# Kernel optimization log

Measured on AMD Instinct MI355X. Metric: run time of the kernel, lower is better.

The kernel has to match this reference:

```python
import jax, jax.numpy as jnp
import numpy as np

SHAPE0 = (256, 256)   # top pyramid level (h, w)
SIGMA = 3.0
EPS = 1e-3
BATCH = 128
N_CHAN = 3
N_LEVELS = 4
N_PIX = sum((SHAPE0[0] >> i) * (SHAPE0[1] >> i) for i in range(N_LEVELS))  # 87040


def _gauss_lum_kernel(sigma):
    # 2D Gaussian times RGB luminance weights -> HWIO kernel (kh, kw, 3, 1)
    s = int(np.ceil(2 * sigma))
    u = np.linspace(-s, s, 2 * s + 1)
    g = np.exp(-(u[:, None] ** 2 + u[None, :] ** 2) / (2 * sigma ** 2)) / (2 * np.pi * sigma ** 2)
    w = np.array([0.2989, 0.587, 0.114])
    k = (g[:, :, None, None] * w[None, None, :, None]).astype(np.float32)
    return jnp.asarray(k)


def _conv_same(x, k):
    # NHWC conv with zero 'SAME' padding; equivalent to the original
    # pad(s) + SAME conv + center crop (net effect is SAME with zero pad).
    return jax.lax.conv_general_dilated(
        x, k, window_strides=(1, 1), padding='SAME',
        dimension_numbers=('NHWC', 'HWIO', 'NHWC'))


def setup_inputs() -> dict:
    key = jax.random.key(0)
    x = jax.random.uniform(key, (BATCH, N_PIX, N_CHAN), dtype=jnp.float32)
    return {"x": x}


def reference(x):
    k = _gauss_lum_kernel(SIGMA)
    n_pix, nc = x.shape[1], x.shape[2]
    h, w = SHAPE0
    outs = []
    i = 0
    while i + h * w <= n_pix:  # static Python loop over pyramid levels
        xi = x[:, i:i + h * w, :].reshape(-1, h, w, nc)          # (B,h,w,3)
        lum = _conv_same(xi, k)                                   # (B,h,w,1)
        dens = _conv_same(jnp.ones((1, h, w, nc), x.dtype), k)    # (1,h,w,1), input-independent
        outs.append((xi / (lum / dens + EPS)).reshape(-1, h * w, nc))
        i += h * w
        h //= 2
        w //= 2
    return jnp.concatenate(outs, axis=1)  # packed pyramid (B, n_pix, 3)
```

## Files before the change

kernel.cpp:

```cpp
#include <hip/hip_runtime.h>


#define NPIX   87040
#define EPSV   1e-3f
#define WSUM   0.9999f
#define TW     64
#define TH     16
#define RAD    6
#define LW     80
#define LWP    84
#define RCP    68
#define LH     28
#define NG     (LH * 20)
#define NBLK   11008
#define NXCD   8
#define CHUNK  (NBLK / NXCD)

__device__ __constant__ float G1[13] = {
    0.01799699f, 0.03315904f, 0.05467002f, 0.08065689f, 0.10648267f,
    0.12579441f, 0.13298076f, 0.12579441f, 0.10648267f, 0.08065689f,
    0.05467002f, 0.03315904f, 0.01799699f
};
__device__ __constant__ float PRE[14] = {
    0.00000000f, 0.01799699f, 0.05115603f, 0.10582605f, 0.18648294f,
    0.29296561f, 0.41876002f, 0.55174078f, 0.67753519f, 0.78401786f,
    0.86467475f, 0.91934477f, 0.95250381f, 0.97050080f
};

__global__ __launch_bounds__(256)
void mslln_kernel(const float* __restrict__ x, float* __restrict__ out) {
    __shared__ float s_mem[LH * LWP];
    __shared__ float s_rc[LH][RCP];
    float (*s_lum)[LWP]   = (float(*)[LWP])s_mem;
    float (*s_scale)[RCP] = (float(*)[RCP])s_mem;

    const int bphys = blockIdx.x;
    const int bid   = (bphys & (NXCD - 1)) * CHUNK + (bphys >> 3);
    const int t     = threadIdx.x;

    int img, tl, txlog, h, off;
    if (bid < 8192)       { img = bid >> 6;                 tl = bid & 63; txlog = 2; h = 256; off = 0;     }
    else if (bid < 10240) { int r = bid - 8192;  img = r >> 4; tl = r & 15; txlog = 1; h = 128; off = 65536; }
    else if (bid < 10752) { int r = bid - 10240; img = r >> 2; tl = r & 3;  txlog = 0; h = 64;  off = 81920; }
    else                  { int r = bid - 10752; img = r >> 1; tl = r & 1;  txlog = 0; h = 32;  off = 86016; }
    const int w   = h;
    const int tx0 = (tl & ((1 << txlog) - 1)) << 6;
    const int ty0 = (tl >> txlog) << 4;

    const float* __restrict__ xb = x   + (size_t)img * (NPIX * 3) + (size_t)off * 3;
    float*       __restrict__ ob = out + (size_t)img * (NPIX * 3) + (size_t)off * 3;

#pragma unroll
    for (int k = 0; k < 3; k++) {
        unsigned i = t + k * 256;
        if (i < NG) {
            int gr  = i / 20;
            int gc  = i - gr * 20;
            int gy  = ty0 + gr - RAD;
            int gx0 = tx0 + (gc << 2) - 8;
            float4 f0 = {0,0,0,0}, f1 = {0,0,0,0}, f2 = {0,0,0,0};
            if (gy >= 0 && gy < h) {
                if (gx0 >= 0 && gx0 + 3 < w) {
                    const float4* p = (const float4*)(xb + ((size_t)gy * w + gx0) * 3);
                    f0 = p[0]; f1 = p[1]; f2 = p[2];
                } else {
                    float v[12];
#pragma unroll
                    for (int c = 0; c < 12; c++) v[c] = 0.f;
#pragma unroll
                    for (int c = 0; c < 4; c++) {
                        int gx = gx0 + c;
                        if (gx >= 0 && gx < w) {
                            const float* s = xb + ((size_t)gy * w + gx) * 3;
                            v[3*c] = s[0]; v[3*c+1] = s[1]; v[3*c+2] = s[2];
                        }
                    }
                    f0 = make_float4(v[0], v[1], v[2],  v[3]);
                    f1 = make_float4(v[4], v[5], v[6],  v[7]);
                    f2 = make_float4(v[8], v[9], v[10], v[11]);
                }
            }
            float l0 = 0.2989f*f0.x + 0.587f*f0.y + 0.114f*f0.z;
            float l1 = 0.2989f*f0.w + 0.587f*f1.x + 0.114f*f1.y;
            float l2 = 0.2989f*f1.z + 0.587f*f1.w + 0.114f*f2.x;
            float l3 = 0.2989f*f2.y + 0.587f*f2.z + 0.114f*f2.w;
            *(float4*)&s_lum[gr][gc << 2] = make_float4(l0, l1, l2, l3);
        }
    }
    __syncthreads();

    const int p4_gr  = t >> 4;
    const int p4_gc  = t & 15;
    const int p4_gx0 = tx0 + (p4_gc << 2);
    float4 f0p = {0,0,0,0}, f1p = {0,0,0,0}, f2p = {0,0,0,0};
    if (p4_gx0 < w) {
        const float4* p = (const float4*)(xb + ((size_t)(ty0 + p4_gr) * w + p4_gx0) * 3);
        f0p = p[0]; f1p = p[1]; f2p = p[2];
    }

#pragma unroll
    for (int k = 0; k < 2; k++) {
        int gi = t + (k << 8);
        if (gi < 448) {
            int r  = gi >> 4;
            int c4 = (gi & 15) << 2;
            float a[20];
#pragma unroll
            for (int m = 0; m < 5; m++)
                *(float4*)&a[m << 2] = *(const float4*)&s_lum[r][c4 + (m << 2)];
            float s0 = 0.f, s1 = 0.f, s2 = 0.f, s3 = 0.f;
#pragma unroll
            for (int j = 0; j < 13; j++) {
                float gj = G1[j];
                s0 += a[2 + j] * gj;
                s1 += a[3 + j] * gj;
                s2 += a[4 + j] * gj;
                s3 += a[5 + j] * gj;
            }
            *(float4*)&s_rc[r][c4] = make_float4(s0, s1, s2, s3);
        }
    }
    __syncthreads();

    {
        int ly  = t >> 4;
        int lx4 = (t & 15) << 2;
        if (tx0 + lx4 < w) {
            float4 acc = {0.f, 0.f, 0.f, 0.f};
#pragma unroll
            for (int j = 0; j < 13; j++) {
                float4 v = *(const float4*)&s_rc[ly + j][lx4];
                float gj = G1[j];
                acc.x += v.x * gj; acc.y += v.y * gj;
                acc.z += v.z * gj; acc.w += v.w * gj;
            }
            int gy = ty0 + ly;
            int ylo = min(RAD, gy), yhi = min(RAD, h - 1 - gy);
            float Sy = PRE[RAD + yhi + 1] - PRE[RAD - ylo];
            float4 sc;
#pragma unroll
            for (int d = 0; d < 4; d++) {
                int gx = tx0 + lx4 + d;
                int xlo = min(RAD, gx), xhi = min(RAD, w - 1 - gx);
                float Sx = PRE[RAD + xhi + 1] - PRE[RAD - xlo];
                float dens = WSUM * Sy * Sx;
                float s = (d == 0) ? acc.x : (d == 1) ? acc.y : (d == 2) ? acc.z : acc.w;
                float r = dens / (s + EPSV * dens);
                if (d == 0) sc.x = r; else if (d == 1) sc.y = r;
                else if (d == 2) sc.z = r; else sc.w = r;
            }
            *(float4*)&s_scale[ly][lx4] = sc;
        }
    }
    __syncthreads();

    if (p4_gx0 < w) {
        float4 sc = *(const float4*)&s_scale[p4_gr][p4_gc << 2];
        f0p.x *= sc.x; f0p.y *= sc.x; f0p.z *= sc.x; f0p.w *= sc.y;
        f1p.x *= sc.y; f1p.y *= sc.y; f1p.z *= sc.z; f1p.w *= sc.z;
        f2p.x *= sc.z; f2p.y *= sc.w; f2p.z *= sc.w; f2p.w *= sc.w;
        float4* q = (float4*)(ob + ((size_t)(ty0 + p4_gr) * w + p4_gx0) * 3);
        q[0] = f0p; q[1] = f1p; q[2] = f2p;
    }
}

extern "C" void kernel_launch(void* const* d_in, const int* in_sizes, int n_in,
                              void* d_out, int out_size, void* d_ws, size_t ws_size,
                              hipStream_t stream) {
    const float* x = (const float*)d_in[0];
    float* out = (float*)d_out;
    mslln_kernel<<<NBLK, 256, 0, stream>>>(x, out);
}
```

Before: 243.9 us.

## Convert kernel to persistent blocks looping over tiles per XCD

```diff
diff --git a/kernel.cpp b/kernel.cpp
--- a/kernel.cpp
+++ b/kernel.cpp
@@ -4,17 +4,15 @@
 #define NPIX   87040
 #define EPSV   1e-3f
 #define WSUM   0.9999f
-#define TW     64
-#define TH     16
 #define RAD    6
 #define LW     80
 #define LWP    84
 #define RCP    68
 #define LH     28
 #define NG     (LH * 20)
-#define NBLK   11008
 #define NXCD   8
-#define CHUNK  (NBLK / NXCD)
+#define TPX    1376
+#define NRES   2048
 
 __device__ __constant__ float G1[13] = {
     0.01799699f, 0.03315904f, 0.05467002f, 0.08065689f, 0.10648267f,
@@ -27,6 +25,20 @@
     0.86467475f, 0.91934477f, 0.95250381f, 0.97050080f
 };
 
+__device__ __forceinline__ void decode_tile(int bid, const float* x, float* out,
+    const float*& xb, float*& ob, int& w, int& tx0, int& ty0) {
+    int img, tl, txlog, h, off;
+    if (bid < 8192)       { img = bid >> 6;                 tl = bid & 63; txlog = 2; h = 256; off = 0;     }
+    else if (bid < 10240) { int r = bid - 8192;  img = r >> 4; tl = r & 15; txlog = 1; h = 128; off = 65536; }
+    else if (bid < 10752) { int r = bid - 10240; img = r >> 2; tl = r & 3;  txlog = 0; h = 64;  off = 81920; }
+    else                  { int r = bid - 10752; img = r >> 1; tl = r & 1;  txlog = 0; h = 32;  off = 86016; }
+    w   = h;
+    tx0 = (tl & ((1 << txlog) - 1)) << 6;
+    ty0 = (tl >> txlog) << 4;
+    xb  = x   + (size_t)img * (NPIX * 3) + (size_t)off * 3;
+    ob  = out + (size_t)img * (NPIX * 3) + (size_t)off * 3;
+}
+
 __global__ __launch_bounds__(256)
 void mslln_kernel(const float* __restrict__ x, float* __restrict__ out) {
     __shared__ float s_mem[LH * LWP];
@@ -34,103 +46,102 @@
     float (*s_lum)[LWP]   = (float(*)[LWP])s_mem;
     float (*s_scale)[RCP] = (float(*)[RCP])s_mem;
 
-    const int bphys = blockIdx.x;
-    const int bid   = (bphys & (NXCD - 1)) * CHUNK + (bphys >> 3);
-    const int t     = threadIdx.x;
+    const int b    = blockIdx.x;
+    const int xcd  = b & (NXCD - 1);
+    const int slot = b >> 3;
+    const int t    = threadIdx.x;
+    const int nj   = (slot < TPX - 5 * 256) ? 6 : 5;
 
-    int img, tl, txlog, h, off;
-    if (bid < 8192)       { img = bid >> 6;                 tl = bid & 63; txlog = 2; h = 256; off = 0;     }
-    else if (bid < 10240) { int r = bid - 8192;  img = r >> 4; tl = r & 15; txlog = 1; h = 128; off = 65536; }
-    else if (bid < 10752) { int r = bid - 10240; img = r >> 2; tl = r & 3;  txlog = 0; h = 64;  off = 81920; }
-    else                  { int r = bid - 10752; img = r >> 1; tl = r & 1;  txlog = 0; h = 32;  off = 86016; }
-    const int w   = h;
-    const int tx0 = (tl & ((1 << txlog) - 1)) << 6;
-    const int ty0 = (tl >> txlog) << 4;
+    int g_r[3], g_c[3];
+#pragma unroll
+    for (int k = 0; k < 3; k++) {
+        int i = t + (k << 8);
+        int gr = i / 20;
+        g_r[k] = gr; g_c[k] = i - gr * 20;
+    }
+    const int ly  = t >> 4;
+    const int lx4 = (t & 15) << 2;
 
-    const float* __restrict__ xb = x   + (size_t)img * (NPIX * 3) + (size_t)off * 3;
-    float*       __restrict__ ob = out + (size_t)img * (NPIX * 3) + (size_t)off * 3;
+    for (int j = 0; j < nj; j++) {
+        const int bid = xcd * TPX + (j << 8) + slot;
+        const float* xb; float* ob; int w, tx0, ty0;
+        decode_tile(bid, x, out, xb, ob, w, tx0, ty0);
+        const int h = w;
 
 #pragma unroll
-    for (int k = 0; k < 3; k++) {
-        unsigned i = t + k * 256;
-        if (i < NG) {
-            int gr  = i / 20;
-            int gc  = i - gr * 20;
-            int gy  = ty0 + gr - RAD;
-            int gx0 = tx0 + (gc << 2) - 8;
-            float4 f0 = {0,0,0,0}, f1 = {0,0,0,0}, f2 = {0,0,0,0};
-            if (gy >= 0 && gy < h) {
-                if (gx0 >= 0 && gx0 + 3 < w) {
-                    const float4* p = (const float4*)(xb + ((size_t)gy * w + gx0) * 3);
-                    f0 = p[0]; f1 = p[1]; f2 = p[2];
-                } else {
-                    float v[12];
+        for (int k = 0; k < 3; k++) {
+            if (t + (k << 8) < NG) {
+                int gr  = g_r[k];
+                int gc  = g_c[k];
+                int gy  = ty0 + gr - RAD;
+                int gx0 = tx0 + (gc << 2) - 8;
+                float4 f0 = {0,0,0,0}, f1 = {0,0,0,0}, f2 = {0,0,0,0};
+                if (gy >= 0 && gy < h) {
+                    if (gx0 >= 0 && gx0 + 3 < w) {
+                        const float4* p = (const float4*)(xb + ((size_t)gy * w + gx0) * 3);
+                        f0 = p[0]; f1 = p[1]; f2 = p[2];
+                    } else {
+                        float v[12];
 #pragma unroll
-                    for (int c = 0; c < 12; c++) v[c] = 0.f;
+                        for (int c = 0; c < 12; c++) v[c] = 0.f;
 #pragma unroll
-                    for (int c = 0; c < 4; c++) {
-                        int gx = gx0 + c;
-                        if (gx >= 0 && gx < w) {
-                            const float* s = xb + ((size_t)gy * w + gx) * 3;
-                            v[3*c] = s[0]; v[3*c+1] = s[1]; v[3*c+2] = s[2];
+                        for (int c = 0; c < 4; c++) {
+                            int gx = gx0 + c;
+                            if (gx >= 0 && gx < w) {
+                                const float* s = xb + ((size_t)gy * w + gx) * 3;
+                                v[3*c] = s[0]; v[3*c+1] = s[1]; v[3*c+2] = s[2];
+                            }
                         }
+                        f0 = make_float4(v[0], v[1], v[2],  v[3]);
+                        f1 = make_float4(v[4], v[5], v[6],  v[7]);
+                        f2 = make_float4(v[8], v[9], v[10], v[11]);
                     }
-                    f0 = make_float4(v[0], v[1], v[2],  v[3]);
-                    f1 = make_float4(v[4], v[5], v[6],  v[7]);
-                    f2 = make_float4(v[8], v[9], v[10], v[11]);
                 }
+                float l0 = 0.2989f*f0.x + 0.587f*f0.y + 0.114f*f0.z;
+                float l1 = 0.2989f*f0.w + 0.587f*f1.x + 0.114f*f1.y;
+                float l2 = 0.2989f*f1.z + 0.587f*f1.w + 0.114f*f2.x;
+                float l3 = 0.2989f*f2.y + 0.587f*f2.z + 0.114f*f2.w;
+                *(float4*)&s_lum[gr][gc << 2] = make_float4(l0, l1, l2, l3);
             }
-            float l0 = 0.2989f*f0.x + 0.587f*f0.y + 0.114f*f0.z;
-            float l1 = 0.2989f*f0.w + 0.587f*f1.x + 0.114f*f1.y;
-            float l2 = 0.2989f*f1.z + 0.587f*f1.w + 0.114f*f2.x;
-            float l3 = 0.2989f*f2.y + 0.587f*f2.z + 0.114f*f2.w;
-            *(float4*)&s_lum[gr][gc << 2] = make_float4(l0, l1, l2, l3);
         }
-    }
-    __syncthreads();
+        __syncthreads();
 
-    const int p4_gr  = t >> 4;
-    const int p4_gc  = t & 15;
-    const int p4_gx0 = tx0 + (p4_gc << 2);
-    float4 f0p = {0,0,0,0}, f1p = {0,0,0,0}, f2p = {0,0,0,0};
-    if (p4_gx0 < w) {
-        const float4* p = (const float4*)(xb + ((size_t)(ty0 + p4_gr) * w + p4_gx0) * 3);
-        f0p = p[0]; f1p = p[1]; f2p = p[2];
-    }
+        float4 f0p = {0,0,0,0}, f1p = {0,0,0,0}, f2p = {0,0,0,0};
+        if (tx0 + lx4 < w) {
+            const float4* p = (const float4*)(xb + ((size_t)(ty0 + ly) * w + tx0 + lx4) * 3);
+            f0p = p[0]; f1p = p[1]; f2p = p[2];
+        }
 
 #pragma unroll
-    for (int k = 0; k < 2; k++) {
-        int gi = t + (k << 8);
-        if (gi < 448) {
-            int r  = gi >> 4;
-            int c4 = (gi & 15) << 2;
-            float a[20];
+        for (int k2 = 0; k2 < 2; k2++) {
+            int gi = t + (k2 << 8);
+            if (gi < 448) {
+                int r  = gi >> 4;
+                int c4 = (gi & 15) << 2;
+                float a[20];
 #pragma unroll
-            for (int m = 0; m < 5; m++)
-                *(float4*)&a[m << 2] = *(const float4*)&s_lum[r][c4 + (m << 2)];
-            float s0 = 0.f, s1 = 0.f, s2 = 0.f, s3 = 0.f;
+                for (int m = 0; m < 5; m++)
+                    *(float4*)&a[m << 2] = *(const float4*)&s_lum[r][c4 + (m << 2)];
+                float s0 = 0.f, s1 = 0.f, s2 = 0.f, s3 = 0.f;
 #pragma unroll
-            for (int j = 0; j < 13; j++) {
-                float gj = G1[j];
-                s0 += a[2 + j] * gj;
-                s1 += a[3 + j] * gj;
-                s2 += a[4 + j] * gj;
-                s3 += a[5 + j] * gj;
+                for (int jj = 0; jj < 13; jj++) {
+                    float gj = G1[jj];
+                    s0 += a[2 + jj] * gj;
+                    s1 += a[3 + jj] * gj;
+                    s2 += a[4 + jj] * gj;
+                    s3 += a[5 + jj] * gj;
+                }
+                *(float4*)&s_rc[r][c4] = make_float4(s0, s1, s2, s3);
             }
-            *(float4*)&s_rc[r][c4] = make_float4(s0, s1, s2, s3);
         }
-    }
-    __syncthreads();
+        __syncthreads();
 
-    {
-        int ly  = t >> 4;
-        int lx4 = (t & 15) << 2;
         if (tx0 + lx4 < w) {
             float4 acc = {0.f, 0.f, 0.f, 0.f};
 #pragma unroll
-            for (int j = 0; j < 13; j++) {
-                float4 v = *(const float4*)&s_rc[ly + j][lx4];
-                float gj = G1[j];
+            for (int jj = 0; jj < 13; jj++) {
+                float4 v = *(const float4*)&s_rc[ly + jj][lx4];
+                float gj = G1[jj];
                 acc.x += v.x * gj; acc.y += v.y * gj;
                 acc.z += v.z * gj; acc.w += v.w * gj;
             }
@@ -151,16 +162,17 @@
             }
             *(float4*)&s_scale[ly][lx4] = sc;
         }
-    }
-    __syncthreads();
+        __syncthreads();
 
-    if (p4_gx0 < w) {
-        float4 sc = *(const float4*)&s_scale[p4_gr][p4_gc << 2];
-        f0p.x *= sc.x; f0p.y *= sc.x; f0p.z *= sc.x; f0p.w *= sc.y;
-        f1p.x *= sc.y; f1p.y *= sc.y; f1p.z *= sc.z; f1p.w *= sc.z;
-        f2p.x *= sc.z; f2p.y *= sc.w; f2p.z *= sc.w; f2p.w *= sc.w;
-        float4* q = (float4*)(ob + ((size_t)(ty0 + p4_gr) * w + p4_gx0) * 3);
-        q[0] = f0p; q[1] = f1p; q[2] = f2p;
+        if (tx0 + lx4 < w) {
+            float4 sc = *(const float4*)&s_scale[ly][lx4];
+            f0p.x *= sc.x; f0p.y *= sc.x; f0p.z *= sc.x; f0p.w *= sc.y;
+            f1p.x *= sc.y; f1p.y *= sc.y; f1p.z *= sc.z; f1p.w *= sc.z;
+            f2p.x *= sc.z; f2p.y *= sc.w; f2p.z *= sc.w; f2p.w *= sc.w;
+            float4* q = (float4*)(ob + ((size_t)(ty0 + ly) * w + tx0 + lx4) * 3);
+            q[0] = f0p; q[1] = f1p; q[2] = f2p;
+        }
+        __syncthreads();
     }
 }
 
@@ -169,5 +181,5 @@
                               hipStream_t stream) {
     const float* x = (const float*)d_in[0];
     float* out = (float*)d_out;
-    mslln_kernel<<<NBLK, 256, 0, stream>>>(x, out);
+    mslln_kernel<<<NRES, 256, 0, stream>>>(x, out);
 }
```

Measured after the change: 262.0 us. 1.07x slower.
